# Optimization experiments

Measured on AMD Instinct MI355X. Metric: run time of the kernel, lower is better.

Reference implementation:

```python
import jax, jax.numpy as jnp
import numpy as np

B, N, DX = 2, 65536, 3
E, H, D, NT = 128, 8, 16, 8
PHI_H, FF_H = 64, 512
PPU = (24.0, 24.0)
MARGIN = (0.1, 0.1)
TIME_DIM = 0


def _ln(x, g, b):
    m = x.mean(-1, keepdims=True)
    v = x.var(-1, keepdims=True)
    return (x - m) / jnp.sqrt(v + 1e-5) * g + b


def _cumcount(idx):
    # for each element, its occurrence count among earlier elements with same value
    n = idx.shape[0]
    order = jnp.argsort(idx)
    s = idx[order]
    is_start = jnp.concatenate([jnp.ones((1,), bool), s[1:] != s[:-1]])
    pos = jnp.arange(n)
    start = jax.lax.cummax(jnp.where(is_start, pos, 0), axis=0)
    return jnp.zeros((n,), jnp.int32).at[order].set((pos - start).astype(jnp.int32))


def _grid_assign(xb, gmin, gmax, grid_shape):
    # k=1 nearest gridded neighbour exploiting regular grid spacing
    gs = jnp.asarray(grid_shape, xb.dtype)
    spacing = (gmax - gmin) / (gs - 1.0)
    multi = jnp.clip(jnp.floor((xb - gmin) / spacing + 0.5), 0.0, gs - 1.0).astype(jnp.int32)
    strides = np.concatenate([np.cumprod(np.asarray(grid_shape[::-1]))[::-1][1:], np.array([1])]).astype(np.int32)
    return (multi * jnp.asarray(strides)).sum(-1)


def _grid_bounds(x):
    spatial = [i for i in range(DX) if i != TIME_DIM]
    lo = [float(jnp.min(x[:, :, i])) - MARGIN[j] for j, i in enumerate(spatial)]
    hi = [float(jnp.max(x[:, :, i])) + MARGIN[j] for j, i in enumerate(spatial)]
    ppd = [int((h - l) * PPU[j]) for j, (l, h) in enumerate(zip(lo, hi))]
    return lo, hi, ppd


def _build_x_grid(lo, hi, ppd, time_grid, b):
    axes = [jnp.linspace(l, h, n) for l, h, n in zip(lo, hi, ppd)]
    mesh = jnp.stack(jnp.meshgrid(*axes, indexing='ij'), -1)  # [n0,n1,2]
    nt = time_grid.shape[1]
    xg = jnp.broadcast_to(mesh[None, None], (b, nt) + tuple(ppd) + (len(ppd),))
    tg = jnp.broadcast_to(time_grid[:, :, None, None], (b, nt) + tuple(ppd))
    return jnp.concatenate([tg[..., None], xg], -1)  # time feature at index 0


def _te_mhca(zq, zk, xq, xk, mask, ln1_g, ln1_b, ln2_g, ln2_b, Wq, Wk, Wv, Wo, bo, pw1, pb1, pw2, pb2, fw1, fb1, fw2, fb2):
    # translation-equivariant masked cross-attention; zq [G,1,E], zk [G,P1,E]
    G, P1, _ = zk.shape
    zqn = _ln(zq, ln1_g, ln1_b)
    zkn = _ln(zk, ln1_g, ln1_b)
    q = (zqn @ Wq).reshape(G, 1, H, D).transpose(0, 2, 1, 3)
    k = (zkn @ Wk).reshape(G, P1, H, D).transpose(0, 2, 1, 3)
    v = (zkn @ Wv).reshape(G, P1, H, D).transpose(0, 2, 1, 3)
    dots = jnp.einsum('ghqd,ghkd->ghqk', q, k) / jnp.sqrt(jnp.asarray(D, q.dtype))
    diff = xq[:, :, None, :] - xk[:, None, :, :]  # [G,1,P1,DX] translation-invariant
    te = jax.nn.gelu(diff @ pw1 + pb1) @ pw2 + pb2  # [G,1,P1,H]
    dots = dots + te.transpose(0, 3, 1, 2)
    dots = jnp.where(mask[:, None, :, :], dots, -1e30)
    attn = jax.nn.softmax(dots, -1)
    out = jnp.einsum('ghqk,ghkd->ghqd', attn, v).transpose(0, 2, 1, 3).reshape(G, 1, H * D)
    zq = zq + out @ Wo + bo
    zq = zq + (jax.nn.gelu(_ln(zq, ln2_g, ln2_b) @ fw1 + fb1) @ fw2 + fb2)
    xq_new = xq - jnp.einsum('ghqk,gqkd->gqd', attn, diff) / H  # update pseudo-locations
    return zq, xq_new


def setup_inputs():
    key = jax.random.key(0)
    ks = jax.random.split(key, 12)
    s = 0.02
    return {
        'x': jax.random.uniform(ks[0], (B, N, DX), jnp.float32),
        'z': jax.random.normal(ks[1], (B, N, E), jnp.float32),
        'time_grid': jnp.broadcast_to(jnp.linspace(0.0, 1.0, NT), (B, NT)).astype(jnp.float32),
        'latent': jax.random.normal(ks[2], (E,), jnp.float32),
        'ln1_g': jnp.ones((E,), jnp.float32), 'ln1_b': jnp.zeros((E,), jnp.float32),
        'ln2_g': jnp.ones((E,), jnp.float32), 'ln2_b': jnp.zeros((E,), jnp.float32),
        'Wq': s * jax.random.normal(ks[3], (E, H * D), jnp.float32),
        'Wk': s * jax.random.normal(ks[4], (E, H * D), jnp.float32),
        'Wv': s * jax.random.normal(ks[5], (E, H * D), jnp.float32),
        'Wo': s * jax.random.normal(ks[6], (H * D, E), jnp.float32),
        'bo': jnp.zeros((E,), jnp.float32),
        'pw1': s * jax.random.normal(ks[7], (DX, PHI_H), jnp.float32),
        'pb1': jnp.zeros((PHI_H,), jnp.float32),
        'pw2': s * jax.random.normal(ks[8], (PHI_H, H), jnp.float32),
        'pb2': jnp.zeros((H,), jnp.float32),
        'fw1': s * jax.random.normal(ks[9], (E, FF_H), jnp.float32),
        'fb1': jnp.zeros((FF_H,), jnp.float32),
        'fw2': s * jax.random.normal(ks[10], (FF_H, E), jnp.float32),
        'fb2': jnp.zeros((E,), jnp.float32),
    }


def reference(x, z, time_grid, latent, ln1_g, ln1_b, ln2_g, ln2_b, Wq, Wk, Wv, Wo, bo, pw1, pb1, pw2, pb2, fw1, fb1, fw2, fb2):
    b, n, dx = x.shape
    lo, hi, ppd = _grid_bounds(x)
    x_grid = _build_x_grid(lo, hi, ppd, time_grid, b)  # [b, nt, n0, n1, dx]
    grid_shape = x_grid.shape[1:-1]
    m = int(np.prod(grid_shape))
    xgf = x_grid.reshape(b, m, dx)
    gmin, gmax = xgf.min(1), xgf.max(1)
    nearest = jax.vmap(lambda xb, a, c: _grid_assign(xb, a, c, grid_shape))(x, gmin, gmax)  # [b, n]
    cum = jax.vmap(_cumcount)(nearest)
    p = int(jnp.max(cum)) + 1  # max points per cell (dynamic in torch too)
    zgf = jnp.broadcast_to(latent, (b, m, E))
    bidx = jnp.arange(b)[:, None]

    def scatter(vals, grid_vals):
        d = vals.shape[-1]
        buf = jnp.zeros((b, m, p, d), vals.dtype).at[bidx, nearest, cum].set(vals)
        return jnp.concatenate([grid_vals[:, :, None, :], buf], 2).reshape(b * m, p + 1, d)

    jx = scatter(x, xgf)
    jz = scatter(z, zgf)
    mask = jnp.zeros((b, m, p), bool).at[bidx, nearest, cum].set(True)
    mask = jnp.concatenate([jnp.ones((b, m, 1), bool), mask], 2).reshape(b * m, 1, p + 1)
    zq = zgf.reshape(b * m, 1, E)
    xq = xgf.reshape(b * m, 1, dx)
    zq, xq = _te_mhca(zq, jz, xq, jx, mask, ln1_g, ln1_b, ln2_g, ln2_b, Wq, Wk, Wv, Wo, bo, pw1, pb1, pw2, pb2, fw1, fb1, fw2, fb2)
    z_grid = zq.reshape((b,) + grid_shape + (E,))
    x_grid_out = xq.reshape((b,) + grid_shape + (dx,))
    return x_grid_out, z_grid
```

## Files before the change

kernel.cpp:

```cpp
#include <hip/hip_runtime.h>
#include <hip/hip_bf16.h>

#define EE 128
#define HH 8
#define DDIM 16
#define NTG 8
#define CAP 64
#define PB 16
#define FFH 512
#define PHIH 64


struct GridParams {
  int n0, n1;
  float lo0f, hi0f, lo1f, hi1f;
  float sp0, sp1;
  float tg0, spt;
};

__device__ __forceinline__ unsigned fenc(float f) {
  unsigned u = __float_as_uint(f);
  return (u & 0x80000000u) ? ~u : (u | 0x80000000u);
}
__device__ __forceinline__ float fdec(unsigned u) {
  unsigned v = (u & 0x80000000u) ? (u ^ 0x80000000u) : ~u;
  return __uint_as_float(v);
}

__device__ __forceinline__ float gelu_f(float x) {
  const float c = 0.7978845608028654f;
  float inner = c * (x + 0.044715f * x * x * x);
  return x * (0.5f * (1.0f + tanhf(inner)));
}

__device__ __forceinline__ int cell_of(const float* __restrict__ x, const GridParams* __restrict__ gp,
                                       int p, int N_, int m, int G) {
  float x0 = x[(size_t)p * 3], x1 = x[(size_t)p * 3 + 1], x2 = x[(size_t)p * 3 + 2];
  int n0 = gp->n0, n1 = gp->n1;
  float u0 = floorf((x0 - gp->tg0) / gp->spt + 0.5f);
  u0 = fminf(fmaxf(u0, 0.0f), 7.0f);
  float u1 = floorf((x1 - gp->lo0f) / gp->sp0 + 0.5f);
  u1 = fminf(fmaxf(u1, 0.0f), (float)(n0 - 1));
  float u2 = floorf((x2 - gp->lo1f) / gp->sp1 + 0.5f);
  u2 = fminf(fmaxf(u2, 0.0f), (float)(n1 - 1));
  int it = (int)u0, i0 = (int)u1, i1 = (int)u2;
  int b = p / N_;
  int g = b * m + (it * n0 + i0) * n1 + i1;
  if (g < 0) g = 0;
  if (g >= G) g = G - 1;
  return g;
}

__global__ void k_init(unsigned* mm, int* counts, int* cursor, int G) {
  int i = blockIdx.x * blockDim.x + threadIdx.x;
  if (i < G) { counts[i] = 0; cursor[i] = 0; }
  if (i == 0) { mm[0] = 0xFFFFFFFFu; mm[1] = 0xFFFFFFFFu; mm[2] = 0u; mm[3] = 0u; }
}

__global__ __launch_bounds__(256) void k_minmax(const float* __restrict__ x, int BN, unsigned* mm) {
  __shared__ float s0[256], s1[256], s2[256], s3[256];
  int t = threadIdx.x;
  float mn1 = 3.4e38f, mn2 = 3.4e38f, mx1 = -3.4e38f, mx2 = -3.4e38f;
  for (int p = blockIdx.x * 256 + t; p < BN; p += gridDim.x * 256) {
    float a = x[(size_t)p * 3 + 1], b = x[(size_t)p * 3 + 2];
    mn1 = fminf(mn1, a); mx1 = fmaxf(mx1, a);
    mn2 = fminf(mn2, b); mx2 = fmaxf(mx2, b);
  }
  s0[t] = mn1; s1[t] = mx1; s2[t] = mn2; s3[t] = mx2;
  __syncthreads();
  for (int off = 128; off >= 1; off >>= 1) {
    if (t < off) {
      s0[t] = fminf(s0[t], s0[t + off]); s1[t] = fmaxf(s1[t], s1[t + off]);
      s2[t] = fminf(s2[t], s2[t + off]); s3[t] = fmaxf(s3[t], s3[t + off]);
    }
    __syncthreads();
  }
  if (t == 0) {
    atomicMin(&mm[0], fenc(s0[0])); atomicMax(&mm[2], fenc(s1[0]));
    atomicMin(&mm[1], fenc(s2[0])); atomicMax(&mm[3], fenc(s3[0]));
  }
}

__global__ __launch_bounds__(64) void k_bounds(const unsigned* mm, const float* __restrict__ tgrid,
                                               GridParams* gp) {
  if (threadIdx.x != 0 || blockIdx.x != 0) return;
  float mn1 = fdec(mm[0]), mx1 = fdec(mm[2]);
  float mn2 = fdec(mm[1]), mx2 = fdec(mm[3]);
  double lo0 = (double)mn1 - 0.1, hi0 = (double)mx1 + 0.1;
  double lo1 = (double)mn2 - 0.1, hi1 = (double)mx2 + 0.1;
  int n0 = (int)((hi0 - lo0) * 24.0);
  int n1 = (int)((hi1 - lo1) * 24.0);
  if (n0 < 2) n0 = 2;
  if (n1 < 2) n1 = 2;
  gp->n0 = n0; gp->n1 = n1;
  float lo0f = (float)lo0, hi0f = (float)hi0, lo1f = (float)lo1, hi1f = (float)hi1;
  gp->lo0f = lo0f; gp->hi0f = hi0f; gp->lo1f = lo1f; gp->hi1f = hi1f;
  gp->sp0 = (hi0f - lo0f) / (float)(n0 - 1);
  gp->sp1 = (hi1f - lo1f) / (float)(n1 - 1);
  float t0 = tgrid[0], t7 = tgrid[NTG - 1];
  gp->tg0 = t0; gp->spt = (t7 - t0) / 7.0f;
}

__global__ __launch_bounds__(128) void k_precompute(
    const float* __restrict__ latent, const float* __restrict__ ln1g, const float* __restrict__ ln1b,
    const float* __restrict__ Wq, const float* __restrict__ Wk, const float* __restrict__ Wv,
    const float* __restrict__ pb1, const float* __restrict__ pw2, const float* __restrict__ pb2,
    float* qvec, float* v0g, float* dot0g, float* qWg) {
  __shared__ float sbuf[EE], zqn[EE], qls[EE], k0[EE], h64[PHIH], stat[2];
  int t = threadIdx.x;
  float lat = latent[t];
  sbuf[t] = lat; __syncthreads();
  for (int off = 64; off >= 1; off >>= 1) { if (t < off) sbuf[t] += sbuf[t + off]; __syncthreads(); }
  if (t == 0) stat[0] = sbuf[0] * (1.0f / 128.0f);
  __syncthreads();
  float dv = lat - stat[0];
  sbuf[t] = dv * dv; __syncthreads();
  for (int off = 64; off >= 1; off >>= 1) { if (t < off) sbuf[t] += sbuf[t + off]; __syncthreads(); }
  if (t == 0) stat[1] = sqrtf(sbuf[0] * (1.0f / 128.0f) + 1e-5f);
  __syncthreads();
  zqn[t] = (lat - stat[0]) / stat[1] * ln1g[t] + ln1b[t];
  __syncthreads();
  float q = 0, k = 0, v = 0;
  for (int e = 0; e < EE; ++e) {
    float zn = zqn[e];
    q += zn * Wq[e * EE + t];
    k += zn * Wk[e * EE + t];
    v += zn * Wv[e * EE + t];
  }
  qvec[t] = q; v0g[t] = v; qls[t] = q; k0[t] = k;
  __syncthreads();
  for (int h = 0; h < HH; ++h) {
    float s = 0;
    #pragma unroll
    for (int d = 0; d < DDIM; ++d) s += qls[h * DDIM + d] * Wk[t * EE + h * DDIM + d];
    qWg[h * EE + t] = 0.25f * s;
  }
  if (t < PHIH) h64[t] = gelu_f(pb1[t]);
  __syncthreads();
  if (t < HH) {
    float s = 0;
    for (int d = 0; d < DDIM; ++d) s += qls[t * DDIM + d] * k0[t * DDIM + d];
    s *= 0.25f;
    float te = pb2[t];
    for (int u = 0; u < PHIH; ++u) te += h64[u] * pw2[u * HH + t];
    dot0g[t] = s + te;
  }
}

__global__ __launch_bounds__(256) void k_assign(
    const float* __restrict__ x, const GridParams* __restrict__ gp,
    int* __restrict__ counts, int BN, int N_, int m, int G) {
  int p = blockIdx.x * 256 + threadIdx.x;
  if (p >= BN) return;
  int g = cell_of(x, gp, p, N_, m, G);
  atomicAdd(&counts[g], 1);
}

__global__ __launch_bounds__(1024) void k_scan(const int* __restrict__ counts,
                                               int* __restrict__ offsets, int G) {
  __shared__ int part[1024];
  int t = threadIdx.x;
  int chunk = (G + 1023) / 1024;
  int lo = t * chunk, hi = lo + chunk; if (hi > G) hi = G; if (lo > G) lo = G;
  int s = 0;
  for (int i = lo; i < hi; ++i) s += counts[i];
  part[t] = s;
  __syncthreads();
  for (int off = 1; off < 1024; off <<= 1) {
    int v = (t >= off) ? part[t - off] : 0;
    __syncthreads();
    part[t] += v;
    __syncthreads();
  }
  int run = (t == 0) ? 0 : part[t - 1];
  for (int i = lo; i < hi; ++i) { offsets[i] = run; run += counts[i]; }
}

__global__ __launch_bounds__(256) void k_scatter(
    const float* __restrict__ x, const GridParams* __restrict__ gp,
    const int* __restrict__ offsets, int* __restrict__ cursor,
    int* __restrict__ compact, int BN, int N_, int m, int G) {
  int p = blockIdx.x * 256 + threadIdx.x;
  if (p >= BN) return;
  int g = cell_of(x, gp, p, N_, m, G);
  int r = atomicAdd(&cursor[g], 1);
  int idx = offsets[g] + r;
  if (idx >= 0 && idx < BN) compact[idx] = p;
}

__global__ __launch_bounds__(128) void k_cell(
    const float* __restrict__ x, const float* __restrict__ z,
    const float* __restrict__ tgrid, const float* __restrict__ latent,
    const float* __restrict__ ln1g, const float* __restrict__ ln1b,
    const float* __restrict__ Wv, const float* __restrict__ Wo, const float* __restrict__ bo,
    const float* __restrict__ pw1, const float* __restrict__ pb1,
    const float* __restrict__ pw2, const float* __restrict__ pb2,
    const float* __restrict__ qWg, const float* __restrict__ v0g, const float* __restrict__ dot0g,
    const GridParams* __restrict__ gp,
    const int* __restrict__ counts, const int* __restrict__ offsets,
    const int* __restrict__ compact,
    float* __restrict__ outx, float* __restrict__ outz, int m, int BN) {
  __shared__ __align__(16) float zb[PB][132];
  __shared__ __align__(16) float hbuf[PB][68];
  __shared__ __align__(16) float pw2T[HH][68];
  __shared__ __align__(16) float wsm[PB][8];
  __shared__ float dotb[CAP][9];
  __shared__ float diffb[CAP][3];
  __shared__ float meanl[PB], invl[PB];
  __shared__ float mh[HH], lh[HH], sch[HH];
  __shared__ __align__(16) float osh[EE];
  __shared__ float asum[CAP];
  __shared__ float xqs[3];

  int t = threadIdx.x;
  int cell = blockIdx.x;
  int b = cell / m, c = cell % m;
  int n0 = gp->n0, n1 = gp->n1;
  int nn = n0 * n1;
  int it = (nn > 0) ? (c / nn) : 0;
  int r2 = (nn > 0) ? (c % nn) : 0;
  int i0 = (n1 > 0) ? (r2 / n1) : 0;
  int i1 = (n1 > 0) ? (r2 % n1) : 0;
  int cnt = counts[cell]; if (cnt > CAP) cnt = CAP; if (cnt < 0) cnt = 0;
  int start = offsets[cell];
  if (start < 0) start = 0;
  if (start > BN - cnt) start = BN - cnt;

  float g1 = ln1g[t], b1 = ln1b[t];
  float zbar[8];
  #pragma unroll
  for (int h = 0; h < 8; ++h) zbar[h] = 0.0f;
  if (t < HH) { mh[t] = dot0g[t]; lh[t] = 1.0f; }
  if (t == 0) {
    int tidx = b * NTG + it;
    if (tidx < 0) tidx = 0;
    if (tidx > 2 * NTG - 1) tidx = 2 * NTG - 1;
    xqs[0] = tgrid[tidx];
    float v;
    if (i0 == n0 - 1) v = gp->hi0f;
    else v = __fadd_rn(gp->lo0f, __fmul_rn((float)i0, gp->sp0));
    xqs[1] = v;
    if (i1 == n1 - 1) v = gp->hi1f;
    else v = __fadd_rn(gp->lo1f, __fmul_rn((float)i1, gp->sp1));
    xqs[2] = v;
  }
  for (int w = t; w < PHIH * HH; w += 128) pw2T[w & 7][w >> 3] = pw2[w];
  __syncthreads();
  for (int w = t; w < cnt * 3; w += 128) {
    int j = w / 3, d = w % 3;
    int pid = compact[start + j];
    diffb[j][d] = (pid >= 0 && pid < BN) ? (xqs[d] - x[(size_t)pid * 3 + d]) : 0.0f;
  }
  __syncthreads();

  for (int jb = 0; jb < cnt; jb += PB) {
    int nb = min(PB, cnt - jb);
    #pragma unroll
    for (int pp = 0; pp < PB; ++pp) {
      float zval = 0.0f;
      if (pp < nb) {
        int pid = compact[start + jb + pp];
        if (pid >= 0 && pid < BN) zval = z[(size_t)pid * EE + t];
      }
      zb[pp][t] = zval;
    }
    __syncthreads();
    {
      int pp = t >> 3, sub = t & 7;
      float s = 0;
      #pragma unroll
      for (int k2 = 0; k2 < 16; ++k2) s += zb[pp][sub + 8 * k2];
      s += __shfl_xor(s, 1); s += __shfl_xor(s, 2); s += __shfl_xor(s, 4);
      float mean = s * (1.0f / 128.0f);
      float v = 0;
      #pragma unroll
      for (int k2 = 0; k2 < 16; ++k2) { float d = zb[pp][sub + 8 * k2] - mean; v += d * d; }
      v += __shfl_xor(v, 1); v += __shfl_xor(v, 2); v += __shfl_xor(v, 4);
      if (sub == 0) { meanl[pp] = mean; invl[pp] = 1.0f / sqrtf(v * (1.0f / 128.0f) + 1e-5f); }
    }
    __syncthreads();
    #pragma unroll
    for (int pp = 0; pp < PB; ++pp)
      zb[pp][t] = (zb[pp][t] - meanl[pp]) * invl[pp] * g1 + b1;
    for (int w = t; w < PB * PHIH; w += 128) {
      int pp = w >> 6, u = w & 63;
      int j = jb + pp;
      float d0 = 0, d1 = 0, d2 = 0;
      if (j < cnt) { d0 = diffb[j][0]; d1 = diffb[j][1]; d2 = diffb[j][2]; }
      float hv = pb1[u] + d0 * pw1[u] + d1 * pw1[PHIH + u] + d2 * pw1[2 * PHIH + u];
      hbuf[pp][u] = gelu_f(hv);
    }
    __syncthreads();
    {
      int pp = t >> 3, h = t & 7;
      float dacc = 0;
      #pragma unroll
      for (int e4 = 0; e4 < 32; ++e4) {
        float4 zn4 = *(const float4*)&zb[pp][e4 * 4];
        float4 qw4 = *(const float4*)&qWg[h * EE + e4 * 4];
        dacc += zn4.x * qw4.x + zn4.y * qw4.y + zn4.z * qw4.z + zn4.w * qw4.w;
      }
      float te = pb2[h];
      #pragma unroll
      for (int u4 = 0; u4 < 16; ++u4) {
        float4 hb = *(const float4*)&hbuf[pp][u4 * 4];
        float4 p2 = *(const float4*)&pw2T[h][u4 * 4];
        te += hb.x * p2.x + hb.y * p2.y + hb.z * p2.z + hb.w * p2.w;
      }
      if (pp < nb) dotb[jb + pp][h] = dacc + te;
    }
    __syncthreads();
    if (t < HH) {
      float mold = mh[t], mb = mold;
      for (int pp = 0; pp < nb; ++pp) mb = fmaxf(mb, dotb[jb + pp][t]);
      float sc = expf(mold - mb);
      float ls = lh[t] * sc;
      for (int pp = 0; pp < nb; ++pp) {
        float w = expf(dotb[jb + pp][t] - mb);
        wsm[pp][t] = w;
        ls += w;
      }
      mh[t] = mb; lh[t] = ls; sch[t] = sc;
    }
    __syncthreads();
    {
      #pragma unroll
      for (int h = 0; h < 8; ++h) zbar[h] *= sch[h];
      for (int pp = 0; pp < nb; ++pp) {
        float znv = zb[pp][t];
        float4 wa = *(const float4*)&wsm[pp][0];
        float4 wb = *(const float4*)&wsm[pp][4];
        zbar[0] += wa.x * znv; zbar[1] += wa.y * znv; zbar[2] += wa.z * znv; zbar[3] += wa.w * znv;
        zbar[4] += wb.x * znv; zbar[5] += wb.y * znv; zbar[6] += wb.z * znv; zbar[7] += wb.w * znv;
      }
    }
    __syncthreads();
  }

  float* zbl = &hbuf[0][0];
  #pragma unroll
  for (int h = 0; h < 8; ++h) zbl[h * EE + t] = zbar[h];
  __syncthreads();
  int hh = t >> 4;
  float w0 = expf(dot0g[hh] - mh[hh]) / lh[hh];
  float osum = 0.0f;
  for (int e4 = 0; e4 < 32; ++e4) {
    int e = e4 * 4;
    float4 zb4 = *(const float4*)&zbl[hh * EE + e];
    osum += zb4.x * Wv[(e + 0) * EE + t] + zb4.y * Wv[(e + 1) * EE + t]
          + zb4.z * Wv[(e + 2) * EE + t] + zb4.w * Wv[(e + 3) * EE + t];
  }
  osh[t] = w0 * v0g[t] + osum / lh[hh];
  if (t < cnt) {
    float s = 0;
    #pragma unroll
    for (int h2 = 0; h2 < HH; ++h2)
      s += expf(dotb[t][h2] - mh[h2]) / lh[h2];
    asum[t] = s;
  }
  __syncthreads();
  float acc = 0;
  for (int e4 = 0; e4 < 32; ++e4) {
    int e = e4 * 4;
    float4 o4 = *(const float4*)&osh[e];
    acc += o4.x * Wo[(e + 0) * EE + t] + o4.y * Wo[(e + 1) * EE + t]
         + o4.z * Wo[(e + 2) * EE + t] + o4.w * Wo[(e + 3) * EE + t];
  }
  float zm = latent[t] + acc + bo[t];
  outz[(size_t)cell * EE + t] = zm;
  if (t < 3) {
    float a = 0;
    for (int j = 0; j < cnt; ++j) a += asum[j] * diffb[j][t];
    outx[(size_t)cell * 3 + t] = xqs[t] - a * (1.0f / 8.0f);
  }
}

__global__ __launch_bounds__(512) void k_ffn(
    const float* __restrict__ ln2g, const float* __restrict__ ln2b,
    const float* __restrict__ fw1, const float* __restrict__ fb1,
    const float* __restrict__ fw2, const float* __restrict__ fb2,
    float* __restrict__ outz, int G) {
  __shared__ float zn[8][EE];
  __shared__ float zr[8][EE];
  __shared__ float gh[8][FFH];
  __shared__ float mv[8], sv[8];
  int t = threadIdx.x;
  int base = blockIdx.x * 8;
  for (int w = t; w < 8 * EE; w += 512) {
    int r = w >> 7, e = w & 127;
    int cell = base + r;
    float v = (cell < G) ? outz[(size_t)cell * EE + e] : 0.0f;
    zn[r][e] = v; zr[r][e] = v;
  }
  __syncthreads();
  {
    int r = t >> 6, lane = t & 63;
    float s = zn[r][lane] + zn[r][lane + 64];
    s += __shfl_xor(s, 1); s += __shfl_xor(s, 2); s += __shfl_xor(s, 4);
    s += __shfl_xor(s, 8); s += __shfl_xor(s, 16); s += __shfl_xor(s, 32);
    float mean = s * (1.0f / 128.0f);
    float d0 = zn[r][lane] - mean, d1 = zn[r][lane + 64] - mean;
    float v = d0 * d0 + d1 * d1;
    v += __shfl_xor(v, 1); v += __shfl_xor(v, 2); v += __shfl_xor(v, 4);
    v += __shfl_xor(v, 8); v += __shfl_xor(v, 16); v += __shfl_xor(v, 32);
    if (lane == 0) { mv[r] = mean; sv[r] = sqrtf(v * (1.0f / 128.0f) + 1e-5f); }
  }
  __syncthreads();
  for (int w = t; w < 8 * EE; w += 512) {
    int r = w >> 7, e = w & 127;
    zn[r][e] = (zn[r][e] - mv[r]) / sv[r] * ln2g[e] + ln2b[e];
  }
  __syncthreads();
  {
    int j = t;
    float acc[8];
    #pragma unroll
    for (int r = 0; r < 8; ++r) acc[r] = 0;
    for (int e = 0; e < EE; ++e) {
      float w = fw1[e * FFH + j];
      #pragma unroll
      for (int r = 0; r < 8; ++r) acc[r] += zn[r][e] * w;
    }
    float fb = fb1[j];
    #pragma unroll
    for (int r = 0; r < 8; ++r) gh[r][j] = gelu_f(acc[r] + fb);
  }
  __syncthreads();
  {
    int e = t & 127; int rb = (t >> 7) * 2;
    float a2[2];
    a2[0] = 0; a2[1] = 0;
    for (int j = 0; j < FFH; ++j) {
      float w = fw2[j * EE + e];
      a2[0] += gh[rb + 0][j] * w;
      a2[1] += gh[rb + 1][j] * w;
    }
    #pragma unroll
    for (int rr = 0; rr < 2; ++rr) {
      int cell = base + rb + rr;
      if (cell < G) outz[(size_t)cell * EE + e] = zr[rb + rr][e] + (a2[rr] + fb2[e]);
    }
  }
}

extern "C" void kernel_launch(void* const* d_in, const int* in_sizes, int n_in,
                              void* d_out, int out_size, void* d_ws, size_t ws_size,
                              hipStream_t stream) {
  const float* x     = (const float*)d_in[0];
  const float* z     = (const float*)d_in[1];
  const float* tgrid = (const float*)d_in[2];
  const float* latent= (const float*)d_in[3];
  const float* ln1g  = (const float*)d_in[4];
  const float* ln1b  = (const float*)d_in[5];
  const float* ln2g  = (const float*)d_in[6];
  const float* ln2b  = (const float*)d_in[7];
  const float* Wq    = (const float*)d_in[8];
  const float* Wk    = (const float*)d_in[9];
  const float* Wv    = (const float*)d_in[10];
  const float* Wo    = (const float*)d_in[11];
  const float* bo    = (const float*)d_in[12];
  const float* pw1   = (const float*)d_in[13];
  const float* pb1   = (const float*)d_in[14];
  const float* pw2   = (const float*)d_in[15];
  const float* pb2   = (const float*)d_in[16];
  const float* fw1   = (const float*)d_in[17];
  const float* fb1   = (const float*)d_in[18];
  const float* fw2   = (const float*)d_in[19];
  const float* fb2   = (const float*)d_in[20];
  (void)n_in; (void)ws_size;

  int Bn = in_sizes[2] / NTG;
  int BN = in_sizes[0] / 3;
  int N_ = BN / Bn;
  int G  = out_size / 131;
  int m  = G / Bn;

  char* ws = (char*)d_ws;
  unsigned* mm    = (unsigned*)ws;
  GridParams* gp  = (GridParams*)(ws + 64);
  float* qvec     = (float*)(ws + 128);
  float* v0g      = (float*)(ws + 128 + 512);
  float* dot0g    = (float*)(ws + 128 + 1024);
  float* qWg      = (float*)(ws + 2048);
  size_t off = 8192;
  int* counts     = (int*)(ws + off); off += (size_t)G * 4;
  int* offsets    = (int*)(ws + off); off += (size_t)G * 4;
  int* cursor     = (int*)(ws + off); off += (size_t)G * 4;
  int* compact    = (int*)(ws + off); off += (size_t)BN * 4;

  float* outx = (float*)d_out;
  float* outz = outx + (size_t)G * 3;

  hipLaunchKernelGGL(k_init, dim3((G + 255) / 256), dim3(256), 0, stream, mm, counts, cursor, G);
  hipLaunchKernelGGL(k_minmax, dim3(256), dim3(256), 0, stream, x, BN, mm);
  hipLaunchKernelGGL(k_bounds, dim3(1), dim3(64), 0, stream, mm, tgrid, gp);
  hipLaunchKernelGGL(k_precompute, dim3(1), dim3(128), 0, stream,
                     latent, ln1g, ln1b, Wq, Wk, Wv, pb1, pw2, pb2, qvec, v0g, dot0g, qWg);
  hipLaunchKernelGGL(k_assign, dim3((BN + 255) / 256), dim3(256), 0, stream,
                     x, gp, counts, BN, N_, m, G);
  hipLaunchKernelGGL(k_scan, dim3(1), dim3(1024), 0, stream, counts, offsets, G);
  hipLaunchKernelGGL(k_scatter, dim3((BN + 255) / 256), dim3(256), 0, stream,
                     x, gp, offsets, cursor, compact, BN, N_, m, G);
  hipLaunchKernelGGL(k_cell, dim3(G), dim3(128), 0, stream,
                     x, z, tgrid, latent, ln1g, ln1b, Wv, Wo, bo,
                     pw1, pb1, pw2, pb2, qWg, v0g, dot0g, gp, counts, offsets, compact,
                     outx, outz, m, BN);
  hipLaunchKernelGGL(k_ffn, dim3((G + 7) / 8), dim3(512), 0, stream,
                     ln2g, ln2b, fw1, fb1, fw2, fb2, outz, G);
}
```

Baseline: 339.8 us.

## Map one wavefront per cell in k_cell and drop block barriers

Each 128-thread block of k_cell now handles two grid cells, one 64-lane wavefront per cell. Each lane owns two embedding channels, and all shared-memory staging is duplicated per wave. This relies on wavefront lockstep execution, so every __syncthreads in the point loop and the epilogue is removed. The point batch size PB drops from 16 to 8 to match the 64-lane layout. The aim is to cut barrier stalls and idle lanes in small cells. The cost is intra-wave LDS communication with no explicit fences, which is correct only if the compiler keeps the store and load order, plus more registers per lane.

After: 363.7 us. 7.0% more time.

```diff
diff --git a/kernel.cpp b/kernel.cpp
--- a/kernel.cpp
+++ b/kernel.cpp
@@ -6,7 +6,7 @@
 #define DDIM 16
 #define NTG 8
 #define CAP 64
-#define PB 16
+#define PB 8
 #define FFH 512
 #define PHIH 64
 
@@ -199,21 +199,23 @@
     const GridParams* __restrict__ gp,
     const int* __restrict__ counts, const int* __restrict__ offsets,
     const int* __restrict__ compact,
-    float* __restrict__ outx, float* __restrict__ outz, int m, int BN) {
-  __shared__ __align__(16) float zb[PB][132];
-  __shared__ __align__(16) float hbuf[PB][68];
-  __shared__ __align__(16) float pw2T[HH][68];
-  __shared__ __align__(16) float wsm[PB][8];
-  __shared__ float dotb[CAP][9];
-  __shared__ float diffb[CAP][3];
-  __shared__ float meanl[PB], invl[PB];
-  __shared__ float mh[HH], lh[HH], sch[HH];
-  __shared__ __align__(16) float osh[EE];
-  __shared__ float asum[CAP];
-  __shared__ float xqs[3];
+    float* __restrict__ outx, float* __restrict__ outz, int m, int BN, int G) {
+  __shared__ __align__(16) float zbS[2][PB * 132];
+  __shared__ __align__(16) float hbS[2][PB][68];
+  __shared__ __align__(16) float pw2TS[2][HH][68];
+  __shared__ __align__(16) float wsmS[2][PB][8];
+  __shared__ __align__(16) float oslS[2][EE];
+  __shared__ float dotbS[2][CAP][9];
+  __shared__ float diffbS[2][CAP][3];
+  __shared__ float mlS[2][PB], ivS[2][PB];
+  __shared__ float mhS[2][HH], lhS[2][HH], schS[2][HH];
+  __shared__ float asumS[2][CAP];
 
   int t = threadIdx.x;
-  int cell = blockIdx.x;
+  int w = t >> 6, l = t & 63;
+  int cell = blockIdx.x * 2 + w;
+  if (cell >= G) return;
+
   int b = cell / m, c = cell % m;
   int n0 = gp->n0, n1 = gp->n1;
   int nn = n0 * n1;
@@ -226,152 +228,163 @@
   if (start < 0) start = 0;
   if (start > BN - cnt) start = BN - cnt;
 
-  float g1 = ln1g[t], b1 = ln1b[t];
-  float zbar[8];
-  #pragma unroll
-  for (int h = 0; h < 8; ++h) zbar[h] = 0.0f;
-  if (t < HH) { mh[t] = dot0g[t]; lh[t] = 1.0f; }
-  if (t == 0) {
+  float xq0, xq1, xq2;
+  {
     int tidx = b * NTG + it;
     if (tidx < 0) tidx = 0;
     if (tidx > 2 * NTG - 1) tidx = 2 * NTG - 1;
-    xqs[0] = tgrid[tidx];
-    float v;
-    if (i0 == n0 - 1) v = gp->hi0f;
-    else v = __fadd_rn(gp->lo0f, __fmul_rn((float)i0, gp->sp0));
-    xqs[1] = v;
-    if (i1 == n1 - 1) v = gp->hi1f;
-    else v = __fadd_rn(gp->lo1f, __fmul_rn((float)i1, gp->sp1));
-    xqs[2] = v;
-  }
-  for (int w = t; w < PHIH * HH; w += 128) pw2T[w & 7][w >> 3] = pw2[w];
-  __syncthreads();
-  for (int w = t; w < cnt * 3; w += 128) {
-    int j = w / 3, d = w % 3;
-    int pid = compact[start + j];
-    diffb[j][d] = (pid >= 0 && pid < BN) ? (xqs[d] - x[(size_t)pid * 3 + d]) : 0.0f;
-  }
-  __syncthreads();
+    xq0 = tgrid[tidx];
+    if (i0 == n0 - 1) xq1 = gp->hi0f;
+    else xq1 = __fadd_rn(gp->lo0f, __fmul_rn((float)i0, gp->sp0));
+    if (i1 == n1 - 1) xq2 = gp->hi1f;
+    else xq2 = __fadd_rn(gp->lo1f, __fmul_rn((float)i1, gp->sp1));
+  }
+  if (l < HH) { mhS[w][l] = dot0g[l]; lhS[w][l] = 1.0f; }
+  for (int w2 = l; w2 < HH * PHIH; w2 += 64) pw2TS[w][w2 & 7][w2 >> 3] = pw2[w2];
+  if (l < cnt) {
+    int pid = compact[start + l];
+    bool ok = (pid >= 0 && pid < BN);
+    diffbS[w][l][0] = ok ? (xq0 - x[(size_t)pid * 3 + 0]) : 0.0f;
+    diffbS[w][l][1] = ok ? (xq1 - x[(size_t)pid * 3 + 1]) : 0.0f;
+    diffbS[w][l][2] = ok ? (xq2 - x[(size_t)pid * 3 + 2]) : 0.0f;
+  }
+
+  float g1a = ln1g[l], b1a = ln1b[l];
+  float g1b = ln1g[l + 64], b1b = ln1b[l + 64];
+  float zbarA[8], zbarB[8];
+  #pragma unroll
+  for (int h = 0; h < 8; ++h) { zbarA[h] = 0.0f; zbarB[h] = 0.0f; }
+  float* zb = zbS[w];
 
   for (int jb = 0; jb < cnt; jb += PB) {
     int nb = min(PB, cnt - jb);
     #pragma unroll
     for (int pp = 0; pp < PB; ++pp) {
-      float zval = 0.0f;
       if (pp < nb) {
         int pid = compact[start + jb + pp];
-        if (pid >= 0 && pid < BN) zval = z[(size_t)pid * EE + t];
+        float a = 0.0f, c2 = 0.0f;
+        if (pid >= 0 && pid < BN) {
+          a  = z[(size_t)pid * EE + l];
+          c2 = z[(size_t)pid * EE + l + 64];
+        }
+        zb[pp * 132 + l] = a;
+        zb[pp * 132 + l + 64] = c2;
       }
-      zb[pp][t] = zval;
-    }
-    __syncthreads();
+    }
     {
-      int pp = t >> 3, sub = t & 7;
+      int pp = l >> 3, sub = l & 7;
       float s = 0;
       #pragma unroll
-      for (int k2 = 0; k2 < 16; ++k2) s += zb[pp][sub + 8 * k2];
+      for (int k2 = 0; k2 < 16; ++k2) s += zb[pp * 132 + sub + 8 * k2];
       s += __shfl_xor(s, 1); s += __shfl_xor(s, 2); s += __shfl_xor(s, 4);
       float mean = s * (1.0f / 128.0f);
       float v = 0;
       #pragma unroll
-      for (int k2 = 0; k2 < 16; ++k2) { float d = zb[pp][sub + 8 * k2] - mean; v += d * d; }
+      for (int k2 = 0; k2 < 16; ++k2) { float d = zb[pp * 132 + sub + 8 * k2] - mean; v += d * d; }
       v += __shfl_xor(v, 1); v += __shfl_xor(v, 2); v += __shfl_xor(v, 4);
-      if (sub == 0) { meanl[pp] = mean; invl[pp] = 1.0f / sqrtf(v * (1.0f / 128.0f) + 1e-5f); }
-    }
-    __syncthreads();
-    #pragma unroll
-    for (int pp = 0; pp < PB; ++pp)
-      zb[pp][t] = (zb[pp][t] - meanl[pp]) * invl[pp] * g1 + b1;
-    for (int w = t; w < PB * PHIH; w += 128) {
-      int pp = w >> 6, u = w & 63;
+      if (sub == 0) { mlS[w][pp] = mean; ivS[w][pp] = 1.0f / sqrtf(v * (1.0f / 128.0f) + 1e-5f); }
+    }
+    #pragma unroll
+    for (int pp = 0; pp < PB; ++pp) {
+      if (pp < nb) {
+        float mean = mlS[w][pp], inv = ivS[w][pp];
+        zb[pp * 132 + l]      = (zb[pp * 132 + l]      - mean) * inv * g1a + b1a;
+        zb[pp * 132 + l + 64] = (zb[pp * 132 + l + 64] - mean) * inv * g1b + b1b;
+      }
+    }
+    for (int w2 = l; w2 < PB * PHIH; w2 += 64) {
+      int pp = w2 >> 6, u = w2 & 63;
       int j = jb + pp;
       float d0 = 0, d1 = 0, d2 = 0;
-      if (j < cnt) { d0 = diffb[j][0]; d1 = diffb[j][1]; d2 = diffb[j][2]; }
+      if (j < cnt) { d0 = diffbS[w][j][0]; d1 = diffbS[w][j][1]; d2 = diffbS[w][j][2]; }
       float hv = pb1[u] + d0 * pw1[u] + d1 * pw1[PHIH + u] + d2 * pw1[2 * PHIH + u];
-      hbuf[pp][u] = gelu_f(hv);
-    }
-    __syncthreads();
+      hbS[w][pp][u] = gelu_f(hv);
+    }
     {
-      int pp = t >> 3, h = t & 7;
+      int pp = l >> 3, h = l & 7;
       float dacc = 0;
       #pragma unroll
       for (int e4 = 0; e4 < 32; ++e4) {
-        float4 zn4 = *(const float4*)&zb[pp][e4 * 4];
+        float4 zn4 = *(const float4*)&zb[pp * 132 + e4 * 4];
         float4 qw4 = *(const float4*)&qWg[h * EE + e4 * 4];
         dacc += zn4.x * qw4.x + zn4.y * qw4.y + zn4.z * qw4.z + zn4.w * qw4.w;
       }
       float te = pb2[h];
       #pragma unroll
       for (int u4 = 0; u4 < 16; ++u4) {
-        float4 hb = *(const float4*)&hbuf[pp][u4 * 4];
-        float4 p2 = *(const float4*)&pw2T[h][u4 * 4];
+        float4 hb = *(const float4*)&hbS[w][pp][u4 * 4];
+        float4 p2 = *(const float4*)&pw2TS[w][h][u4 * 4];
         te += hb.x * p2.x + hb.y * p2.y + hb.z * p2.z + hb.w * p2.w;
       }
-      if (pp < nb) dotb[jb + pp][h] = dacc + te;
-    }
-    __syncthreads();
-    if (t < HH) {
-      float mold = mh[t], mb = mold;
-      for (int pp = 0; pp < nb; ++pp) mb = fmaxf(mb, dotb[jb + pp][t]);
+      if (pp < nb) dotbS[w][jb + pp][h] = dacc + te;
+    }
+    if (l < HH) {
+      float mold = mhS[w][l], mb = mold;
+      for (int pp = 0; pp < nb; ++pp) mb = fmaxf(mb, dotbS[w][jb + pp][l]);
       float sc = expf(mold - mb);
-      float ls = lh[t] * sc;
+      float ls = lhS[w][l] * sc;
       for (int pp = 0; pp < nb; ++pp) {
-        float w = expf(dotb[jb + pp][t] - mb);
-        wsm[pp][t] = w;
-        ls += w;
+        float wv = expf(dotbS[w][jb + pp][l] - mb);
+        wsmS[w][pp][l] = wv;
+        ls += wv;
       }
-      mh[t] = mb; lh[t] = ls; sch[t] = sc;
-    }
-    __syncthreads();
+      mhS[w][l] = mb; lhS[w][l] = ls; schS[w][l] = sc;
+    }
     {
       #pragma unroll
-      for (int h = 0; h < 8; ++h) zbar[h] *= sch[h];
+      for (int h = 0; h < 8; ++h) { float sc = schS[w][h]; zbarA[h] *= sc; zbarB[h] *= sc; }
       for (int pp = 0; pp < nb; ++pp) {
-        float znv = zb[pp][t];
-        float4 wa = *(const float4*)&wsm[pp][0];
-        float4 wb = *(const float4*)&wsm[pp][4];
-        zbar[0] += wa.x * znv; zbar[1] += wa.y * znv; zbar[2] += wa.z * znv; zbar[3] += wa.w * znv;
-        zbar[4] += wb.x * znv; zbar[5] += wb.y * znv; zbar[6] += wb.z * znv; zbar[7] += wb.w * znv;
+        float znA = zb[pp * 132 + l], znB = zb[pp * 132 + l + 64];
+        float4 wa = *(const float4*)&wsmS[w][pp][0];
+        float4 wb = *(const float4*)&wsmS[w][pp][4];
+        zbarA[0] += wa.x * znA; zbarA[1] += wa.y * znA; zbarA[2] += wa.z * znA; zbarA[3] += wa.w * znA;
+        zbarA[4] += wb.x * znA; zbarA[5] += wb.y * znA; zbarA[6] += wb.z * znA; zbarA[7] += wb.w * znA;
+        zbarB[0] += wa.x * znB; zbarB[1] += wa.y * znB; zbarB[2] += wa.z * znB; zbarB[3] += wa.w * znB;
+        zbarB[4] += wb.x * znB; zbarB[5] += wb.y * znB; zbarB[6] += wb.z * znB; zbarB[7] += wb.w * znB;
       }
     }
-    __syncthreads();
-  }
-
-  float* zbl = &hbuf[0][0];
+  }
+
   #pragma unroll
-  for (int h = 0; h < 8; ++h) zbl[h * EE + t] = zbar[h];
-  __syncthreads();
-  int hh = t >> 4;
-  float w0 = expf(dot0g[hh] - mh[hh]) / lh[hh];
-  float osum = 0.0f;
-  for (int e4 = 0; e4 < 32; ++e4) {
-    int e = e4 * 4;
-    float4 zb4 = *(const float4*)&zbl[hh * EE + e];
-    osum += zb4.x * Wv[(e + 0) * EE + t] + zb4.y * Wv[(e + 1) * EE + t]
-          + zb4.z * Wv[(e + 2) * EE + t] + zb4.w * Wv[(e + 3) * EE + t];
-  }
-  osh[t] = w0 * v0g[t] + osum / lh[hh];
-  if (t < cnt) {
+  for (int h = 0; h < 8; ++h) {
+    zb[h * EE + l] = zbarA[h];
+    zb[h * EE + l + 64] = zbarB[h];
+  }
+  if (l < cnt) {
     float s = 0;
     #pragma unroll
     for (int h2 = 0; h2 < HH; ++h2)
-      s += expf(dotb[t][h2] - mh[h2]) / lh[h2];
-    asum[t] = s;
-  }
-  __syncthreads();
-  float acc = 0;
-  for (int e4 = 0; e4 < 32; ++e4) {
-    int e = e4 * 4;
-    float4 o4 = *(const float4*)&osh[e];
-    acc += o4.x * Wo[(e + 0) * EE + t] + o4.y * Wo[(e + 1) * EE + t]
-         + o4.z * Wo[(e + 2) * EE + t] + o4.w * Wo[(e + 3) * EE + t];
-  }
-  float zm = latent[t] + acc + bo[t];
-  outz[(size_t)cell * EE + t] = zm;
-  if (t < 3) {
+      s += expf(dotbS[w][l][h2] - mhS[w][h2]) / lhS[w][h2];
+    asumS[w][l] = s;
+  }
+  {
+    int e0 = l, e1 = l + 64;
+    int h0 = e0 >> 4, h1 = e1 >> 4;
+    float os0 = 0, os1 = 0;
+    for (int ep = 0; ep < EE; ++ep) {
+      os0 += zb[h0 * EE + ep] * Wv[ep * EE + e0];
+      os1 += zb[h1 * EE + ep] * Wv[ep * EE + e1];
+    }
+    float w00 = expf(dot0g[h0] - mhS[w][h0]) / lhS[w][h0];
+    float w01 = expf(dot0g[h1] - mhS[w][h1]) / lhS[w][h1];
+    oslS[w][e0] = w00 * v0g[e0] + os0 / lhS[w][h0];
+    oslS[w][e1] = w01 * v0g[e1] + os1 / lhS[w][h1];
+  }
+  {
+    float acc0 = 0, acc1 = 0;
+    for (int ep = 0; ep < EE; ++ep) {
+      float ov = oslS[w][ep];
+      acc0 += ov * Wo[ep * EE + l];
+      acc1 += ov * Wo[ep * EE + l + 64];
+    }
+    outz[(size_t)cell * EE + l] = latent[l] + acc0 + bo[l];
+    outz[(size_t)cell * EE + l + 64] = latent[l + 64] + acc1 + bo[l + 64];
+  }
+  if (l < 3) {
     float a = 0;
-    for (int j = 0; j < cnt; ++j) a += asum[j] * diffb[j][t];
-    outx[(size_t)cell * 3 + t] = xqs[t] - a * (1.0f / 8.0f);
+    for (int j = 0; j < cnt; ++j) a += asumS[w][j] * diffbS[w][j][l];
+    float xc = (l == 0) ? xq0 : ((l == 1) ? xq1 : xq2);
+    outx[(size_t)cell * 3 + l] = xc - a * (1.0f / 8.0f);
   }
 }
 
@@ -501,10 +514,10 @@
   hipLaunchKernelGGL(k_scan, dim3(1), dim3(1024), 0, stream, counts, offsets, G);
   hipLaunchKernelGGL(k_scatter, dim3((BN + 255) / 256), dim3(256), 0, stream,
                      x, gp, offsets, cursor, compact, BN, N_, m, G);
-  hipLaunchKernelGGL(k_cell, dim3(G), dim3(128), 0, stream,
+  hipLaunchKernelGGL(k_cell, dim3((G + 1) / 2), dim3(128), 0, stream,
                      x, z, tgrid, latent, ln1g, ln1b, Wv, Wo, bo,
                      pw1, pb1, pw2, pb2, qWg, v0g, dot0g, gp, counts, offsets, compact,
-                     outx, outz, m, BN);
+                     outx, outz, m, BN, G);
   hipLaunchKernelGGL(k_ffn, dim3((G + 7) / 8), dim3(512), 0, stream,
                      ln2g, ln2b, fw1, fb1, fw2, fb2, outz, G);
 }
```
